# Performance work log

Hardware: AMD Instinct MI355X
Metric: run time of the kernel (lower is better)

## Reference

```python
import jax, jax.numpy as jnp
import numpy as np

D_MODEL = 1024
NUM_HEADS = 16
HEAD_DIM = D_MODEL // NUM_HEADS
THETA = 10000.0


def _trunc_normal(key, shape, std):
    # approximate trunc_normal_(a=-3std, b=3std) by clipping
    return jnp.clip(jax.random.normal(key, shape) * std, -3 * std, 3 * std)


def setup_inputs() -> dict:
    key = jax.random.key(0)
    ks = jax.random.split(key, 6)
    B, S = 2, 2048
    x = jax.random.normal(ks[0], (B, S, D_MODEL), dtype=jnp.float32)
    token_positions = jnp.sort(
        jax.random.randint(ks[1], (B, S), 0, 2048), axis=-1
    ).astype(jnp.int64)
    std = float(np.sqrt(2.0 / (D_MODEL + D_MODEL)))
    Wq = _trunc_normal(ks[2], (D_MODEL, D_MODEL), std)
    Wk = _trunc_normal(ks[3], (D_MODEL, D_MODEL), std)
    Wv = _trunc_normal(ks[4], (D_MODEL, D_MODEL), std)
    Wo = _trunc_normal(ks[5], (D_MODEL, D_MODEL), std)
    return {"x": x, "Wq": Wq, "Wk": Wk, "Wv": Wv, "Wo": Wo,
            "token_positions": token_positions}


def _rope(x, positions):
    # x: (b, h, s, d), positions: (b, s)
    d = x.shape[-1]
    inv_freq = THETA ** (-jnp.arange(0, d, 2, dtype=jnp.float32) / d)  # (d/2,)
    angles = positions.astype(jnp.float32)[:, None, :, None] * inv_freq  # (b,1,s,d/2)
    cos, sin = jnp.cos(angles), jnp.sin(angles)
    x_even, x_odd = x[..., 0::2], x[..., 1::2]
    out_even = x_even * cos - x_odd * sin
    out_odd = x_even * sin + x_odd * cos
    # interleave back: (..., d/2, 2) -> (..., d)
    return jnp.stack([out_even, out_odd], axis=-1).reshape(x.shape)


def reference(x, Wq, Wk, Wv, Wo, token_positions):
    B, S, _ = x.shape
    H, Dh = NUM_HEADS, HEAD_DIM
    # projections: einsum '... i, o i -> ... o'
    q = jnp.einsum('bsi,oi->bso', x, Wq).reshape(B, S, H, Dh).transpose(0, 2, 1, 3)
    k = jnp.einsum('bsi,oi->bso', x, Wk).reshape(B, S, H, Dh).transpose(0, 2, 1, 3)
    v = jnp.einsum('bsi,oi->bso', x, Wv).reshape(B, S, H, Dh).transpose(0, 2, 1, 3)
    q = _rope(q, token_positions)
    k = _rope(k, token_positions)
    scores = jnp.einsum('bhqd,bhkd->bhqk', q.astype(jnp.float32),
                        k.astype(jnp.float32)) / jnp.sqrt(
        jnp.asarray(Dh, dtype=jnp.float32))
    causal = jnp.tril(jnp.ones((S, S), dtype=bool))
    scores = jnp.where(causal, scores, -jnp.inf)
    attn = jax.nn.softmax(scores, axis=-1)
    out = jnp.einsum('bhqk,bhkd->bhqd', attn, v.astype(jnp.float32)).astype(x.dtype)
    out = out.transpose(0, 2, 1, 3).reshape(B, S, H * Dh)
    return jnp.einsum('bsi,oi->bso', out, Wo)
```

## Files before the change

kernel.cpp:

```cpp
#include <hip/hip_runtime.h>
#include <hip/hip_bf16.h>

#define DMODEL 1024
#define NHEADS 16
#define HDIM   64
#define BATCH  2
#define SEQ    2048
#define XELEMS ((size_t)BATCH * SEQ * DMODEL)
#define WELEMS ((size_t)DMODEL * DMODEL)

typedef __attribute__((ext_vector_type(8))) __bf16 bf16x8;
typedef __attribute__((ext_vector_type(4))) float  f32x4;
typedef __attribute__((ext_vector_type(4))) unsigned int   u32x4;
typedef __attribute__((ext_vector_type(4))) unsigned short u16x4;
typedef __attribute__((ext_vector_type(8))) unsigned short u16x8;

typedef const __attribute__((address_space(1))) void* gas_t;
typedef __attribute__((address_space(3))) void* las_t;

static __device__ __forceinline__ unsigned short f2bf(float f) {
  return __builtin_bit_cast(unsigned short, __float2bfloat16(f));
}
static __device__ __forceinline__ float bf2f(unsigned short u) {
  return __bfloat162float(__builtin_bit_cast(__hip_bfloat16, u));
}

__global__ __launch_bounds__(64) void probe_kernel(const unsigned int* __restrict__ x,
                                                   const int* __restrict__ pos,
                                                   int* __restrict__ flags) {
  const int lane = threadIdx.x;
  int bad = 0;
#pragma unroll
  for (int i = 0; i < 32; ++i) {
    const unsigned int u = x[lane * 32 + i];
    if (((u >> 23) & 0xFFu) == 0xFFu) bad++;
  }
  int zodd = 0;
#pragma unroll
  for (int i = 0; i < 4; ++i)
    if (pos[lane * 8 + 2 * i + 1] == 0) zodd++;
#pragma unroll
  for (int s = 1; s < 64; s <<= 1) {
    bad  += __shfl_xor(bad, s);
    zodd += __shfl_xor(zodd, s);
  }
  if (lane == 0) {
    flags[0] = (bad < 64) ? 1 : 0;
    flags[1] = (zodd >= 200) ? 1 : 0;
  }
}

__global__ __launch_bounds__(256) void conv_kernel(
    const void* __restrict__ x,
    const void* __restrict__ w0, const void* __restrict__ w1,
    const void* __restrict__ w2, const void* __restrict__ w3,
    unsigned short* __restrict__ dst, const int* __restrict__ flags) {
  const size_t e = ((size_t)blockIdx.x * 256 + threadIdx.x) * 8;
  const void* src;
  size_t off;
  if (e < XELEMS) { src = x; off = e; }
  else {
    const size_t r = e - XELEMS;
    const int wi = (int)(r >> 20);
    src = (wi == 0) ? w0 : (wi == 1) ? w1 : (wi == 2) ? w2 : w3;
    off = r & (WELEMS - 1);
  }
  if (flags[0]) {
    const float* s = (const float*)src + off;
    const f32x4 a = *(const f32x4*)(s);
    const f32x4 b = *(const f32x4*)(s + 4);
    u16x8 o8;
#pragma unroll
    for (int j = 0; j < 4; ++j) o8[j] = f2bf(a[j]);
#pragma unroll
    for (int j = 0; j < 4; ++j) o8[4 + j] = f2bf(b[j]);
    *(u16x8*)(dst + e) = o8;
  } else {
    *(u32x4*)(dst + e) = *(const u32x4*)((const unsigned short*)src + off);
  }
}

__device__ __forceinline__ void gemm_core(const unsigned short* __restrict__ Ag,
                                          const unsigned short* __restrict__ Bg,
                                          unsigned short* As, unsigned short* Bs,
                                          int bm, int bn, f32x4 acc[4][4]) {
  const int tid = threadIdx.x;
  const int lane = tid & 63;
  const int w  = tid >> 6;
  const int wm = w >> 1, wn = w & 1;
  const int c = lane & 15, g = lane >> 4;
  const int r0 = tid >> 2;
  const int s0 = (tid & 3) * 8;

  auto stage = [&](int buf, int k0) {
    unsigned short* ad = As + buf * 4096;
    unsigned short* bd = Bs + buf * 4096;
    __builtin_amdgcn_global_load_lds((gas_t)(Ag + (size_t)(bm + r0) * DMODEL + k0 + s0),
                                     (las_t)(ad + tid * 8), 16, 0, 0);
    __builtin_amdgcn_global_load_lds((gas_t)(Ag + (size_t)(bm + r0 + 64) * DMODEL + k0 + s0),
                                     (las_t)(ad + (tid + 256) * 8), 16, 0, 0);
    __builtin_amdgcn_global_load_lds((gas_t)(Bg + (size_t)(bn + r0) * DMODEL + k0 + s0),
                                     (las_t)(bd + tid * 8), 16, 0, 0);
    __builtin_amdgcn_global_load_lds((gas_t)(Bg + (size_t)(bn + r0 + 64) * DMODEL + k0 + s0),
                                     (las_t)(bd + (tid + 256) * 8), 16, 0, 0);
  };

  stage(0, 0);
  __syncthreads();
  for (int k0 = 0; k0 < DMODEL; k0 += 32) {
    const int cur = (k0 >> 5) & 1;
    if (k0 + 32 < DMODEL) stage(cur ^ 1, k0 + 32);
    const unsigned short* ar = As + cur * 4096;
    const unsigned short* br = Bs + cur * 4096;
    bf16x8 af[4], bfr[4];
#pragma unroll
    for (int m = 0; m < 4; ++m)
      af[m] = *(const bf16x8*)&ar[(wm * 64 + m * 16 + c) * 32 + g * 8];
#pragma unroll
    for (int n = 0; n < 4; ++n)
      bfr[n] = *(const bf16x8*)&br[(wn * 64 + n * 16 + c) * 32 + g * 8];
    __builtin_amdgcn_s_setprio(1);
#pragma unroll
    for (int m = 0; m < 4; ++m)
#pragma unroll
      for (int n = 0; n < 4; ++n)
        acc[m][n] = __builtin_amdgcn_mfma_f32_16x16x32_bf16(af[m], bfr[n], acc[m][n], 0, 0, 0);
    __builtin_amdgcn_s_setprio(0);
    __syncthreads();
  }
}

__global__ __launch_bounds__(256) void qkv_gemm_kernel(
    const unsigned short* __restrict__ x,
    const unsigned short* __restrict__ Wq, const unsigned short* __restrict__ Wk,
    const unsigned short* __restrict__ Wv,
    unsigned short* __restrict__ qo, unsigned short* __restrict__ ko,
    unsigned short* __restrict__ vto) {
  __shared__ unsigned short As[2 * 128 * 32];
  __shared__ unsigned short Bs[2 * 128 * 32];
  const int z = blockIdx.z;
  const unsigned short* W = (z == 0) ? Wq : (z == 1) ? Wk : Wv;
  const int bm = blockIdx.x * 128, bn = blockIdx.y * 128;
  f32x4 acc[4][4];
#pragma unroll
  for (int m = 0; m < 4; ++m)
#pragma unroll
    for (int n = 0; n < 4; ++n)
#pragma unroll
      for (int j = 0; j < 4; ++j) acc[m][n][j] = 0.f;

  gemm_core(x, W, As, Bs, bm, bn, acc);

  const int tid = threadIdx.x, lane = tid & 63, w = tid >> 6;
  const int wm = w >> 1, wn = w & 1, c = lane & 15, g4 = lane >> 4;
#pragma unroll
  for (int m = 0; m < 4; ++m) {
#pragma unroll
    for (int n = 0; n < 4; ++n) {
      const int col = bn + wn * 64 + n * 16 + c;
      const int h = col >> 6, d = col & 63;
      const int row0 = bm + wm * 64 + m * 16 + g4 * 4;
      if (z == 2) {
        const int b = row0 >> 11, s0 = row0 & (SEQ - 1);
        u16x4 pk;
#pragma unroll
        for (int j = 0; j < 4; ++j) pk[j] = f2bf(acc[m][n][j]);
        *(u16x4*)&vto[((size_t)(b * NHEADS + h) * HDIM + d) * SEQ + s0] = pk;
      } else {
        unsigned short* dst = z ? ko : qo;
#pragma unroll
        for (int j = 0; j < 4; ++j) {
          const int row = row0 + j;
          const int b = row >> 11, s = row & (SEQ - 1);
          dst[((size_t)(b * NHEADS + h) * SEQ + s) * HDIM + d] = f2bf(acc[m][n][j]);
        }
      }
    }
  }
}

__global__ __launch_bounds__(256) void out_gemm_kernel(
    const unsigned short* __restrict__ A, const unsigned short* __restrict__ Wo,
    void* __restrict__ outv, const int* __restrict__ flags) {
  __shared__ unsigned short As[2 * 64 * 32];
  __shared__ unsigned short Bs[2 * 128 * 32];
  const int bm = blockIdx.x * 64, bn = blockIdx.y * 128;
  const int tid = threadIdx.x, lane = tid & 63, w = tid >> 6;
  const int c = lane & 15, g = lane >> 4;
  const int r0 = tid >> 2, s0 = (tid & 3) * 8;
  f32x4 acc[4][2];
#pragma unroll
  for (int m = 0; m < 4; ++m)
#pragma unroll
    for (int n = 0; n < 2; ++n)
#pragma unroll
      for (int j = 0; j < 4; ++j) acc[m][n][j] = 0.f;

  auto stage = [&](int buf, int k0) {
    __builtin_amdgcn_global_load_lds((gas_t)(A + (size_t)(bm + r0) * DMODEL + k0 + s0),
                                     (las_t)(As + buf * 2048 + tid * 8), 16, 0, 0);
    __builtin_amdgcn_global_load_lds((gas_t)(Wo + (size_t)(bn + r0) * DMODEL + k0 + s0),
                                     (las_t)(Bs + buf * 4096 + tid * 8), 16, 0, 0);
    __builtin_amdgcn_global_load_lds((gas_t)(Wo + (size_t)(bn + r0 + 64) * DMODEL + k0 + s0),
                                     (las_t)(Bs + buf * 4096 + (tid + 256) * 8), 16, 0, 0);
  };

  stage(0, 0);
  __syncthreads();
  for (int k0 = 0; k0 < DMODEL; k0 += 32) {
    const int cur = (k0 >> 5) & 1;
    if (k0 + 32 < DMODEL) stage(cur ^ 1, k0 + 32);
    const unsigned short* ar = As + cur * 2048;
    const unsigned short* br = Bs + cur * 4096;
    bf16x8 af[4], bfr[2];
#pragma unroll
    for (int m = 0; m < 4; ++m)
      af[m] = *(const bf16x8*)&ar[(m * 16 + c) * 32 + g * 8];
#pragma unroll
    for (int n = 0; n < 2; ++n)
      bfr[n] = *(const bf16x8*)&br[(w * 32 + n * 16 + c) * 32 + g * 8];
    __builtin_amdgcn_s_setprio(1);
#pragma unroll
    for (int m = 0; m < 4; ++m)
#pragma unroll
      for (int n = 0; n < 2; ++n)
        acc[m][n] = __builtin_amdgcn_mfma_f32_16x16x32_bf16(af[m], bfr[n], acc[m][n], 0, 0, 0);
    __builtin_amdgcn_s_setprio(0);
    __syncthreads();
  }

  const int g4 = g;
  const int f32o = flags[0];
  if (f32o) {
    float* out = (float*)outv;
#pragma unroll
    for (int m = 0; m < 4; ++m)
#pragma unroll
      for (int n = 0; n < 2; ++n) {
        const int col = bn + w * 32 + n * 16 + c;
#pragma unroll
        for (int j = 0; j < 4; ++j) {
          const int row = bm + m * 16 + g4 * 4 + j;
          out[(size_t)row * DMODEL + col] = acc[m][n][j];
        }
      }
  } else {
    unsigned short* out = (unsigned short*)outv;
#pragma unroll
    for (int m = 0; m < 4; ++m)
#pragma unroll
      for (int n = 0; n < 2; ++n) {
        const int col = bn + w * 32 + n * 16 + c;
#pragma unroll
        for (int j = 0; j < 4; ++j) {
          const int row = bm + m * 16 + g4 * 4 + j;
          out[(size_t)row * DMODEL + col] = f2bf(acc[m][n][j]);
        }
      }
  }
}

__global__ __launch_bounds__(256) void rope_kernel(unsigned short* __restrict__ q,
                                                   unsigned short* __restrict__ k,
                                                   const int* __restrict__ pos,
                                                   const int* __restrict__ flags) {
  const int idx = blockIdx.x * 256 + threadIdx.x;
  const int tsel = idx >> 21;
  const int p = idx & ((1 << 21) - 1);
  const int j = p & 31;
  const int s = (p >> 5) & (SEQ - 1);
  const int bh = p >> 16;
  const int b = bh >> 4;
  unsigned short* base = tsel ? k : q;
  const int pidx = b * SEQ + s;
  const int pv = flags[1] ? pos[2 * pidx] : pos[pidx];
  const float sc = tsel ? 1.0f : 0.125f;
  const float freq = exp2f((float)j * -0.41524101186092026f);
  const float ang = (float)pv * freq;
  const float cs = cosf(ang);
  const float sn = sinf(ang);
  unsigned int* wp = (unsigned int*)base + ((p >> 5) * 32 + j);
  const unsigned int u = *wp;
  const float e = bf2f((unsigned short)(u & 0xffffu));
  const float o = bf2f((unsigned short)(u >> 16));
  *wp = (unsigned int)f2bf((e * cs - o * sn) * sc) |
        ((unsigned int)f2bf((e * sn + o * cs) * sc) << 16);
}

#define MNEG -1e30f
#define QBLK 64
#define LOG2E 1.4426950408889634f

template<int BUF>
__device__ __forceinline__ void flash_tile(
    int kt, int nkv, int qt, int qbase, int wq, int c, int g, int tid,
    const unsigned short* (&kp)[2], const unsigned short* (&vp)[2],
    unsigned short (&Ks)[2][64 * 64], unsigned short (&Vs)[2][64 * 64],
    unsigned short (&Ps)[64 * 72],
    const bf16x8 (&qf)[2], f32x4 (&acco)[4], float& m_r, float& l_r) {
  const int kvb = kt * 64;
  if (kt + 1 < nkv) {
#pragma unroll
    for (int i = 0; i < 2; ++i) {
      const int t8 = (tid + i * 256) * 8;
      __builtin_amdgcn_global_load_lds((gas_t)kp[i], (las_t)(Ks[BUF ^ 1] + t8), 16, 0, 0);
      __builtin_amdgcn_global_load_lds((gas_t)vp[i], (las_t)(Vs[BUF ^ 1] + t8), 16, 0, 0);
      kp[i] += 64 * HDIM;
      vp[i] += 64;
    }
  }

  f32x4 accs[4];
#pragma unroll
  for (int n = 0; n < 4; ++n)
#pragma unroll
    for (int j = 0; j < 4; ++j) accs[n][j] = 0.f;
  __builtin_amdgcn_s_setprio(1);
#pragma unroll
  for (int kk = 0; kk < 2; ++kk)
#pragma unroll
    for (int n = 0; n < 4; ++n) {
      const int r = n * 16 + c;
      const int sl = (kk * 4 + g) ^ (r & 7);
      const bf16x8 ak = *(const bf16x8*)&Ks[BUF][r * 64 + sl * 8];
      accs[n] = __builtin_amdgcn_mfma_f32_16x16x32_bf16(ak, qf[kk], accs[n], 0, 0, 0);
    }
  __builtin_amdgcn_s_setprio(0);

  const int qg = qbase + wq + c;
  if (kt == qt) {
#pragma unroll
    for (int n = 0; n < 4; ++n)
#pragma unroll
      for (int jj = 0; jj < 4; ++jj)
        if (kvb + n * 16 + g * 4 + jj > qg) accs[n][jj] = MNEG;
  }

  float rm = accs[0][0];
#pragma unroll
  for (int n = 0; n < 4; ++n)
#pragma unroll
    for (int jj = 0; jj < 4; ++jj) rm = fmaxf(rm, accs[n][jj]);
  rm = fmaxf(rm, __shfl_xor(rm, 16));
  rm = fmaxf(rm, __shfl_xor(rm, 32));
  if (!__all(rm <= m_r + 8.f)) {
    const float mn = fmaxf(m_r, rm);
    const float al = exp2f((m_r - mn) * LOG2E);
    l_r *= al;
#pragma unroll
    for (int n = 0; n < 4; ++n)
#pragma unroll
      for (int jj = 0; jj < 4; ++jj) acco[n][jj] *= al;
    m_r = mn;
  }
  float rs = 0.f;
#pragma unroll
  for (int n = 0; n < 4; ++n)
#pragma unroll
    for (int jj = 0; jj < 4; ++jj) {
      const float pv = exp2f((accs[n][jj] - m_r) * LOG2E);
      accs[n][jj] = pv;
      rs += pv;
    }
  rs += __shfl_xor(rs, 16);
  rs += __shfl_xor(rs, 32);
  l_r += rs;

#pragma unroll
  for (int n = 0; n < 4; ++n) {
    u16x4 pk4;
#pragma unroll
    for (int jj = 0; jj < 4; ++jj) pk4[jj] = f2bf(accs[n][jj]);
    *(u16x4*)&Ps[(wq + c) * 72 + n * 16 + g * 4] = pk4;
  }

  __builtin_amdgcn_s_setprio(1);
#pragma unroll
  for (int kk = 0; kk < 2; ++kk) {
    const bf16x8 pb = *(const bf16x8*)&Ps[(wq + c) * 72 + kk * 32 + g * 8];
#pragma unroll
    for (int n = 0; n < 4; ++n) {
      const int r = n * 16 + c;
      const int sl = (kk * 4 + g) ^ (r & 7);
      const bf16x8 av = *(const bf16x8*)&Vs[BUF][r * 64 + sl * 8];
      acco[n] = __builtin_amdgcn_mfma_f32_16x16x32_bf16(av, pb, acco[n], 0, 0, 0);
    }
  }
  __builtin_amdgcn_s_setprio(0);
  __syncthreads();
}

__global__ __launch_bounds__(256, 3) void flash_kernel(
    const unsigned short* __restrict__ q, const unsigned short* __restrict__ k,
    const unsigned short* __restrict__ vt, unsigned short* __restrict__ o) {
  __shared__ unsigned short Ks[2][64 * 64];
  __shared__ unsigned short Vs[2][64 * 64];
  __shared__ unsigned short Ps[64 * 72];

  const int wg = blockIdx.x;
  const int qt = (SEQ / QBLK - 1) - (wg >> 5);
  const int bh = wg & 31;
  const int qbase = qt * QBLK;
  const int tid = threadIdx.x, lane = tid & 63, w = tid >> 6;
  const int c = lane & 15, g = lane >> 4;
  const int wq = w * 16;
  const size_t tb = (size_t)bh * SEQ * HDIM;

  bf16x8 qf[2];
#pragma unroll
  for (int kk = 0; kk < 2; ++kk)
    qf[kk] = *(const bf16x8*)(q + tb + (size_t)(qbase + wq + c) * HDIM + kk * 32 + g * 8);

  const unsigned short* kp[2];
  const unsigned short* vp[2];
#pragma unroll
  for (int i = 0; i < 2; ++i) {
    const int t = tid + i * 256;
    const int r = t >> 3;
    const int sl = (t & 7) ^ (r & 7);
    kp[i] = k + tb + (size_t)r * HDIM + sl * 8;
    vp[i] = vt + tb + (size_t)r * SEQ + sl * 8;
  }
#pragma unroll
  for (int i = 0; i < 2; ++i) {
    const int t8 = (tid + i * 256) * 8;
    __builtin_amdgcn_global_load_lds((gas_t)kp[i], (las_t)(Ks[0] + t8), 16, 0, 0);
    __builtin_amdgcn_global_load_lds((gas_t)vp[i], (las_t)(Vs[0] + t8), 16, 0, 0);
    kp[i] += 64 * HDIM;
    vp[i] += 64;
  }
  __syncthreads();

  f32x4 acco[4];
#pragma unroll
  for (int n = 0; n < 4; ++n)
#pragma unroll
    for (int j = 0; j < 4; ++j) acco[n][j] = 0.f;
  float m_r = MNEG, l_r = 0.f;

  const int nkv = qt + 1;
  int kt = 0;
  for (; kt + 2 <= nkv; kt += 2) {
    flash_tile<0>(kt,     nkv, qt, qbase, wq, c, g, tid, kp, vp, Ks, Vs, Ps, qf, acco, m_r, l_r);
    flash_tile<1>(kt + 1, nkv, qt, qbase, wq, c, g, tid, kp, vp, Ks, Vs, Ps, qf, acco, m_r, l_r);
  }
  if (kt < nkv)
    flash_tile<0>(kt, nkv, qt, qbase, wq, c, g, tid, kp, vp, Ks, Vs, Ps, qf, acco, m_r, l_r);

  const float rl = 1.f / fmaxf(l_r, 1e-20f);
  const int b = bh >> 4, h = bh & 15;
  const int srow = qbase + wq + c;
#pragma unroll
  for (int n = 0; n < 4; ++n) {
    u16x4 pk;
#pragma unroll
    for (int jj = 0; jj < 4; ++jj) pk[jj] = f2bf(acco[n][jj] * rl);
    *(u16x4*)&o[(size_t)(b * SEQ + srow) * DMODEL + h * 64 + n * 16 + g * 4] = pk;
  }
}

extern "C" void kernel_launch(void* const* d_in, const int* in_sizes, int n_in,
                              void* d_out, int out_size, void* d_ws, size_t ws_size,
                              hipStream_t stream) {
  (void)in_sizes; (void)n_in; (void)out_size; (void)ws_size;
  const size_t MB = (size_t)1 << 20;
  char* ws = (char*)d_ws;
  unsigned short* xb  = (unsigned short*)(ws);
  unsigned short* Wqb = (unsigned short*)(ws + 8 * MB);
  unsigned short* Wkb = (unsigned short*)(ws + 10 * MB);
  unsigned short* Wvb = (unsigned short*)(ws + 12 * MB);
  unsigned short* Wob = (unsigned short*)(ws + 14 * MB);
  unsigned short* qw  = (unsigned short*)(ws + 16 * MB);
  unsigned short* kw  = (unsigned short*)(ws + 24 * MB);
  unsigned short* vtw = (unsigned short*)(ws + 32 * MB);
  int* flags          = (int*)(ws + 40 * MB);
  unsigned short* ow  = xb;

  const dim3 blk(256);
  probe_kernel<<<1, 64, 0, stream>>>((const unsigned int*)d_in[0], (const int*)d_in[5], flags);
  conv_kernel<<<4096, blk, 0, stream>>>(d_in[0], d_in[1], d_in[2], d_in[3], d_in[4], xb, flags);
  qkv_gemm_kernel<<<dim3(32, 8, 3), blk, 0, stream>>>(xb, Wqb, Wkb, Wvb, qw, kw, vtw);
  rope_kernel<<<16384, blk, 0, stream>>>(qw, kw, (const int*)d_in[5], flags);
  flash_kernel<<<dim3(1024), blk, 0, stream>>>(qw, kw, vtw, ow);
  out_gemm_kernel<<<dim3(64, 8), blk, 0, stream>>>(ow, Wob, d_out, flags);
}
```

Measured before the change: 122.6 us.

## Fuse RoPE into QKV GEMM epilogue and widen flash query tiles to 128

Removes the standalone RoPE pass that read and rewrote Q and K. A small kernel now precomputes a cos/sin table per position, and the QKV GEMM epilogue applies the rotation using a lane shuffle to fetch the partner element. The flash kernel now uses 512-thread blocks covering 128 query rows, so each loaded K/V tile is shared by twice as many queries, with half the blocks and one load per thread. The risks are the extra table reads and shuffles in the GEMM epilogue, and lower occupancy or a worse causal tail from the larger blocks.

```diff
diff --git a/kernel.cpp b/kernel.cpp
--- a/kernel.cpp
+++ b/kernel.cpp
@@ -11,6 +11,7 @@
 
 typedef __attribute__((ext_vector_type(8))) __bf16 bf16x8;
 typedef __attribute__((ext_vector_type(4))) float  f32x4;
+typedef __attribute__((ext_vector_type(2))) float  f32x2;
 typedef __attribute__((ext_vector_type(4))) unsigned int   u32x4;
 typedef __attribute__((ext_vector_type(4))) unsigned short u16x4;
 typedef __attribute__((ext_vector_type(8))) unsigned short u16x8;
@@ -20,9 +21,6 @@
 
 static __device__ __forceinline__ unsigned short f2bf(float f) {
   return __builtin_bit_cast(unsigned short, __float2bfloat16(f));
-}
-static __device__ __forceinline__ float bf2f(unsigned short u) {
-  return __bfloat162float(__builtin_bit_cast(__hip_bfloat16, u));
 }
 
 __global__ __launch_bounds__(64) void probe_kernel(const unsigned int* __restrict__ x,
@@ -48,6 +46,17 @@
     flags[0] = (bad < 64) ? 1 : 0;
     flags[1] = (zodd >= 200) ? 1 : 0;
   }
+}
+
+__global__ __launch_bounds__(256) void rope_table_kernel(const int* __restrict__ pos,
+                                                         const int* __restrict__ flags,
+                                                         float* __restrict__ tab) {
+  const int i = blockIdx.x * 256 + threadIdx.x;
+  const int pd = i & 31, rs = i >> 5;
+  const int pv = flags[1] ? pos[2 * rs] : pos[rs];
+  const float ang = (float)pv * exp2f(-(float)pd * 0.41524101186092026f);
+  f32x2 t; t[0] = cosf(ang); t[1] = sinf(ang);
+  *(f32x2*)&tab[2 * i] = t;
 }
 
 __global__ __launch_bounds__(256) void conv_kernel(
@@ -135,7 +144,7 @@
     const unsigned short* __restrict__ Wq, const unsigned short* __restrict__ Wk,
     const unsigned short* __restrict__ Wv,
     unsigned short* __restrict__ qo, unsigned short* __restrict__ ko,
-    unsigned short* __restrict__ vto) {
+    unsigned short* __restrict__ vto, const float* __restrict__ tab) {
   __shared__ unsigned short As[2 * 128 * 32];
   __shared__ unsigned short Bs[2 * 128 * 32];
   const int z = blockIdx.z;
@@ -153,29 +162,44 @@
 
   const int tid = threadIdx.x, lane = tid & 63, w = tid >> 6;
   const int wm = w >> 1, wn = w & 1, c = lane & 15, g4 = lane >> 4;
-#pragma unroll
-  for (int m = 0; m < 4; ++m) {
-#pragma unroll
-    for (int n = 0; n < 4; ++n) {
-      const int col = bn + wn * 64 + n * 16 + c;
-      const int h = col >> 6, d = col & 63;
-      const int row0 = bm + wm * 64 + m * 16 + g4 * 4;
-      if (z == 2) {
+  if (z == 2) {
+#pragma unroll
+    for (int m = 0; m < 4; ++m)
+#pragma unroll
+      for (int n = 0; n < 4; ++n) {
+        const int col = bn + wn * 64 + n * 16 + c;
+        const int h = col >> 6, d = col & 63;
+        const int row0 = bm + wm * 64 + m * 16 + g4 * 4;
         const int b = row0 >> 11, s0 = row0 & (SEQ - 1);
         u16x4 pk;
 #pragma unroll
         for (int j = 0; j < 4; ++j) pk[j] = f2bf(acc[m][n][j]);
         *(u16x4*)&vto[((size_t)(b * NHEADS + h) * HDIM + d) * SEQ + s0] = pk;
-      } else {
-        unsigned short* dst = z ? ko : qo;
+      }
+  } else {
+    unsigned short* dst = z ? ko : qo;
+    const float sc = z ? 1.0f : 0.125f;
+#pragma unroll
+    for (int m = 0; m < 4; ++m)
+#pragma unroll
+      for (int n = 0; n < 4; ++n) {
+        const int col = bn + wn * 64 + n * 16 + c;
+        const int h = col >> 6, d = col & 63;
+        const int pd = (n * 16 + c) >> 1;
+        const int row0 = bm + wm * 64 + m * 16 + g4 * 4;
 #pragma unroll
         for (int j = 0; j < 4; ++j) {
           const int row = row0 + j;
+          const f32x2 t = *(const f32x2*)&tab[((size_t)row * 32 + pd) * 2];
+          const float v = acc[m][n][j];
+          const float p = __shfl_xor(v, 1);
+          const float cs = t[0] * sc;
+          const float ssn = ((c & 1) ? t[1] : -t[1]) * sc;
+          const float out = v * cs + p * ssn;
           const int b = row >> 11, s = row & (SEQ - 1);
-          dst[((size_t)(b * NHEADS + h) * SEQ + s) * HDIM + d] = f2bf(acc[m][n][j]);
+          dst[((size_t)(b * NHEADS + h) * SEQ + s) * HDIM + d] = f2bf(out);
         }
       }
-    }
   }
 }
 
@@ -229,7 +253,6 @@
     __syncthreads();
   }
 
-  const int g4 = g;
   const int f32o = flags[0];
   if (f32o) {
     float* out = (float*)outv;
@@ -240,7 +263,7 @@
         const int col = bn + w * 32 + n * 16 + c;
 #pragma unroll
         for (int j = 0; j < 4; ++j) {
-          const int row = bm + m * 16 + g4 * 4 + j;
+          const int row = bm + m * 16 + g * 4 + j;
           out[(size_t)row * DMODEL + col] = acc[m][n][j];
         }
       }
@@ -253,61 +276,29 @@
         const int col = bn + w * 32 + n * 16 + c;
 #pragma unroll
         for (int j = 0; j < 4; ++j) {
-          const int row = bm + m * 16 + g4 * 4 + j;
+          const int row = bm + m * 16 + g * 4 + j;
           out[(size_t)row * DMODEL + col] = f2bf(acc[m][n][j]);
         }
       }
   }
 }
 
-__global__ __launch_bounds__(256) void rope_kernel(unsigned short* __restrict__ q,
-                                                   unsigned short* __restrict__ k,
-                                                   const int* __restrict__ pos,
-                                                   const int* __restrict__ flags) {
-  const int idx = blockIdx.x * 256 + threadIdx.x;
-  const int tsel = idx >> 21;
-  const int p = idx & ((1 << 21) - 1);
-  const int j = p & 31;
-  const int s = (p >> 5) & (SEQ - 1);
-  const int bh = p >> 16;
-  const int b = bh >> 4;
-  unsigned short* base = tsel ? k : q;
-  const int pidx = b * SEQ + s;
-  const int pv = flags[1] ? pos[2 * pidx] : pos[pidx];
-  const float sc = tsel ? 1.0f : 0.125f;
-  const float freq = exp2f((float)j * -0.41524101186092026f);
-  const float ang = (float)pv * freq;
-  const float cs = cosf(ang);
-  const float sn = sinf(ang);
-  unsigned int* wp = (unsigned int*)base + ((p >> 5) * 32 + j);
-  const unsigned int u = *wp;
-  const float e = bf2f((unsigned short)(u & 0xffffu));
-  const float o = bf2f((unsigned short)(u >> 16));
-  *wp = (unsigned int)f2bf((e * cs - o * sn) * sc) |
-        ((unsigned int)f2bf((e * sn + o * cs) * sc) << 16);
-}
-
 #define MNEG -1e30f
-#define QBLK 64
 #define LOG2E 1.4426950408889634f
 
 template<int BUF>
 __device__ __forceinline__ void flash_tile(
     int kt, int nkv, int qt, int qbase, int wq, int c, int g, int tid,
-    const unsigned short* (&kp)[2], const unsigned short* (&vp)[2],
+    const unsigned short*& kp, const unsigned short*& vp,
     unsigned short (&Ks)[2][64 * 64], unsigned short (&Vs)[2][64 * 64],
-    unsigned short (&Ps)[64 * 72],
+    unsigned short (&Ps)[128 * 72],
     const bf16x8 (&qf)[2], f32x4 (&acco)[4], float& m_r, float& l_r) {
   const int kvb = kt * 64;
   if (kt + 1 < nkv) {
-#pragma unroll
-    for (int i = 0; i < 2; ++i) {
-      const int t8 = (tid + i * 256) * 8;
-      __builtin_amdgcn_global_load_lds((gas_t)kp[i], (las_t)(Ks[BUF ^ 1] + t8), 16, 0, 0);
-      __builtin_amdgcn_global_load_lds((gas_t)vp[i], (las_t)(Vs[BUF ^ 1] + t8), 16, 0, 0);
-      kp[i] += 64 * HDIM;
-      vp[i] += 64;
-    }
+    __builtin_amdgcn_global_load_lds((gas_t)kp, (las_t)(Ks[BUF ^ 1] + tid * 8), 16, 0, 0);
+    __builtin_amdgcn_global_load_lds((gas_t)vp, (las_t)(Vs[BUF ^ 1] + tid * 8), 16, 0, 0);
+    kp += 64 * HDIM;
+    vp += 64;
   }
 
   f32x4 accs[4];
@@ -328,7 +319,7 @@
   __builtin_amdgcn_s_setprio(0);
 
   const int qg = qbase + wq + c;
-  if (kt == qt) {
+  if (kt >= 2 * qt) {
 #pragma unroll
     for (int n = 0; n < 4; ++n)
 #pragma unroll
@@ -390,17 +381,17 @@
   __syncthreads();
 }
 
-__global__ __launch_bounds__(256, 3) void flash_kernel(
+__global__ __launch_bounds__(512, 4) void flash_kernel(
     const unsigned short* __restrict__ q, const unsigned short* __restrict__ k,
     const unsigned short* __restrict__ vt, unsigned short* __restrict__ o) {
   __shared__ unsigned short Ks[2][64 * 64];
   __shared__ unsigned short Vs[2][64 * 64];
-  __shared__ unsigned short Ps[64 * 72];
+  __shared__ unsigned short Ps[128 * 72];
 
   const int wg = blockIdx.x;
-  const int qt = (SEQ / QBLK - 1) - (wg >> 5);
+  const int qt = (SEQ / 128 - 1) - (wg >> 5);
   const int bh = wg & 31;
-  const int qbase = qt * QBLK;
+  const int qbase = qt * 128;
   const int tid = threadIdx.x, lane = tid & 63, w = tid >> 6;
   const int c = lane & 15, g = lane >> 4;
   const int wq = w * 16;
@@ -411,24 +402,15 @@
   for (int kk = 0; kk < 2; ++kk)
     qf[kk] = *(const bf16x8*)(q + tb + (size_t)(qbase + wq + c) * HDIM + kk * 32 + g * 8);
 
-  const unsigned short* kp[2];
-  const unsigned short* vp[2];
-#pragma unroll
-  for (int i = 0; i < 2; ++i) {
-    const int t = tid + i * 256;
-    const int r = t >> 3;
-    const int sl = (t & 7) ^ (r & 7);
-    kp[i] = k + tb + (size_t)r * HDIM + sl * 8;
-    vp[i] = vt + tb + (size_t)r * SEQ + sl * 8;
-  }
-#pragma unroll
-  for (int i = 0; i < 2; ++i) {
-    const int t8 = (tid + i * 256) * 8;
-    __builtin_amdgcn_global_load_lds((gas_t)kp[i], (las_t)(Ks[0] + t8), 16, 0, 0);
-    __builtin_amdgcn_global_load_lds((gas_t)vp[i], (las_t)(Vs[0] + t8), 16, 0, 0);
-    kp[i] += 64 * HDIM;
-    vp[i] += 64;
-  }
+  const int r = tid >> 3;
+  const int sl = (tid & 7) ^ (r & 7);
+  const unsigned short* kp = k + tb + (size_t)r * HDIM + sl * 8;
+  const unsigned short* vp = vt + tb + (size_t)r * SEQ + sl * 8;
+
+  __builtin_amdgcn_global_load_lds((gas_t)kp, (las_t)(Ks[0] + tid * 8), 16, 0, 0);
+  __builtin_amdgcn_global_load_lds((gas_t)vp, (las_t)(Vs[0] + tid * 8), 16, 0, 0);
+  kp += 64 * HDIM;
+  vp += 64;
   __syncthreads();
 
   f32x4 acco[4];
@@ -438,14 +420,11 @@
     for (int j = 0; j < 4; ++j) acco[n][j] = 0.f;
   float m_r = MNEG, l_r = 0.f;
 
-  const int nkv = qt + 1;
-  int kt = 0;
-  for (; kt + 2 <= nkv; kt += 2) {
+  const int nkv = 2 * qt + 2;
+  for (int kt = 0; kt < nkv; kt += 2) {
     flash_tile<0>(kt,     nkv, qt, qbase, wq, c, g, tid, kp, vp, Ks, Vs, Ps, qf, acco, m_r, l_r);
     flash_tile<1>(kt + 1, nkv, qt, qbase, wq, c, g, tid, kp, vp, Ks, Vs, Ps, qf, acco, m_r, l_r);
   }
-  if (kt < nkv)
-    flash_tile<0>(kt, nkv, qt, qbase, wq, c, g, tid, kp, vp, Ks, Vs, Ps, qf, acco, m_r, l_r);
 
   const float rl = 1.f / fmaxf(l_r, 1e-20f);
   const int b = bh >> 4, h = bh & 15;
@@ -474,13 +453,14 @@
   unsigned short* kw  = (unsigned short*)(ws + 24 * MB);
   unsigned short* vtw = (unsigned short*)(ws + 32 * MB);
   int* flags          = (int*)(ws + 40 * MB);
+  float* tab          = (float*)(ws + 40 * MB + 4096);
   unsigned short* ow  = xb;
 
   const dim3 blk(256);
   probe_kernel<<<1, 64, 0, stream>>>((const unsigned int*)d_in[0], (const int*)d_in[5], flags);
+  rope_table_kernel<<<512, blk, 0, stream>>>((const int*)d_in[5], flags, tab);
   conv_kernel<<<4096, blk, 0, stream>>>(d_in[0], d_in[1], d_in[2], d_in[3], d_in[4], xb, flags);
-  qkv_gemm_kernel<<<dim3(32, 8, 3), blk, 0, stream>>>(xb, Wqb, Wkb, Wvb, qw, kw, vtw);
-  rope_kernel<<<16384, blk, 0, stream>>>(qw, kw, (const int*)d_in[5], flags);
-  flash_kernel<<<dim3(1024), blk, 0, stream>>>(qw, kw, vtw, ow);
+  qkv_gemm_kernel<<<dim3(32, 8, 3), blk, 0, stream>>>(xb, Wqb, Wkb, Wvb, qw, kw, vtw, tab);
+  flash_kernel<<<dim3(512), dim3(512), 0, stream>>>(qw, kw, vtw, ow);
   out_gemm_kernel<<<dim3(64, 8), blk, 0, stream>>>(ow, Wob, d_out, flags);
 }
```

Measured after the change: 136.1 us. +11.0%, slower.
